# Kernel optimization log

Hardware: AMD Instinct MI355X
Metric: run time of the kernel (lower is better)

Reference implementation:

```python
import jax, jax.numpy as jnp
import numpy as np
from jax import lax

N, T, H, W, E = 512, 10, 40, 40, 8192

def _conv2d(x, w, b):
    y = lax.conv_general_dilated(x, w, (1, 1), 'SAME',
                                 dimension_numbers=('NCHW', 'OIHW', 'NCHW'))
    return y + b[None, :, None, None]

def _bn_per_t(x, g, b, eps=1e-5):
    # x: (N, T, C, H, W); torch training-mode BN stats computed per timestep (loop over t in original)
    mu = x.mean(axis=(0, 3, 4), keepdims=True)
    var = x.var(axis=(0, 3, 4), keepdims=True)
    return g[None, None, :, None, None] * (x - mu) * lax.rsqrt(var + eps) + b[None, None, :, None, None]

def _maxpool2(x):
    return lax.reduce_window(x, -jnp.inf, lax.max, (1, 1, 2, 2), (1, 1, 2, 2), 'VALID')

def _cnn(x, w1, b1, g1, be1, w2, b2, g2, be2):
    # conv3x3 -> BN -> relu -> maxpool2 -> conv3x3 -> BN -> relu -> adaptive avgpool(5,5); x: (N,T,Cin,H,W)
    n, t, c, h, w = x.shape
    y = _conv2d(x.reshape(n * t, c, h, w), w1, b1).reshape(n, t, 16, h, w)
    y = jax.nn.relu(_bn_per_t(y, g1, be1))
    y = _maxpool2(y.reshape(n * t, 16, h, w))
    y = _conv2d(y, w2, b2)
    co = w2.shape[0]
    y = jax.nn.relu(_bn_per_t(y.reshape(n, t, co, h // 2, w // 2), g2, be2))
    k = (h // 2) // 5  # 20 -> 5 is a uniform 4x4 average pool
    y = y.reshape(n, t, co, 5, k, 5, k).mean(axis=(4, 6))
    return y.reshape(n, t, co * 25)

def _sage(x, src, dst, wl, bl, wr):
    # PyG SAGEConv(aggr='max'): lin_l(max-aggregated neighbor feats) + lin_r(x); x: (T,N,F)
    t, n, f = x.shape
    msgs = x[:, src]                                               # (T,E,F) gather
    agg = jnp.full((t, n, f), -jnp.inf, x.dtype).at[:, dst].max(msgs)
    agg = jnp.where(jnp.isfinite(agg), agg, 0.0)                   # isolated nodes -> 0 (PyG convention)
    return jnp.einsum('tnf,of->tno', agg, wl) + bl + jnp.einsum('tnf,of->tno', x, wr)

def _lstm_last(x, wih, whh, bih, bhh):
    # x: (T,N,F); torch gate order i,f,g,o; returns final hidden state h_T
    t, n, _ = x.shape
    hdim = whh.shape[1]
    def step(carry, xt):
        h, c = carry
        z = xt @ wih.T + bih + h @ whh.T + bhh
        i, f, g, o = jnp.split(z, 4, axis=-1)
        c = jax.nn.sigmoid(f) * c + jax.nn.sigmoid(i) * jnp.tanh(g)
        h = jax.nn.sigmoid(o) * jnp.tanh(c)
        return (h, c), None
    init = (jnp.zeros((n, hdim), x.dtype), jnp.zeros((n, hdim), x.dtype))
    (h, _), _ = lax.scan(step, init, x)
    return h

def _forward(veg, cwsi, irrigation, edge_index, vw1, vb1, vg1, vbe1, vw2, vb2, vg2, vbe2,
             cw1, cb1, cg1, cbe1, cw2, cb2, cg2, cbe2, emb,
             s1_wl, s1_bl, s1_wr, s2_wl, s2_bl, s2_wr, wih, whh, bih, bhh, fcw, fcb):
    vfeat = _cnn(veg, vw1, vb1, vg1, vbe1, vw2, vb2, vg2, vbe2)    # (N,T,400)
    cfeat = _cnn(cwsi, cw1, cb1, cg1, cbe1, cw2, cb2, cg2, cbe2)   # (N,T,200)
    ifeat = emb[irrigation]                                        # (N,T,16)
    feats = jnp.concatenate([vfeat, cfeat, ifeat], axis=-1).transpose(1, 0, 2)  # (T,N,616)
    src, dst = edge_index[0], edge_index[1]
    x = jax.nn.relu(_sage(feats, src, dst, s1_wl, s1_bl, s1_wr))
    x = jax.nn.relu(_sage(x, src, dst, s2_wl, s2_bl, s2_wr))       # (T,N,32)
    h = _lstm_last(x, wih, whh, bih, bhh)                          # (N,64)
    return h @ fcw.T + fcb                                         # (N,1)

def setup_inputs():
    key = jax.random.key(0)
    ks = jax.random.split(key, 16)
    w = lambda i, shape: jax.random.normal(ks[i], shape, jnp.float32) * 0.05
    return dict(
        veg=jax.random.normal(ks[0], (N, T, 5, H, W), jnp.float32),
        cwsi=jax.random.normal(ks[1], (N, T, 1, H, W), jnp.float32),
        irrigation=jax.random.randint(ks[2], (N, T), 0, 3, jnp.int32),
        edge_index=jax.random.randint(ks[3], (2, E), 0, N, jnp.int32),
        vw1=w(4, (16, 5, 3, 3)), vb1=jnp.zeros(16), vg1=jnp.ones(16), vbe1=jnp.zeros(16),
        vw2=w(5, (16, 16, 3, 3)), vb2=jnp.zeros(16), vg2=jnp.ones(16), vbe2=jnp.zeros(16),
        cw1=w(6, (16, 1, 3, 3)), cb1=jnp.zeros(16), cg1=jnp.ones(16), cbe1=jnp.zeros(16),
        cw2=w(7, (8, 16, 3, 3)), cb2=jnp.zeros(8), cg2=jnp.ones(8), cbe2=jnp.zeros(8),
        emb=jax.random.normal(ks[8], (3, 16), jnp.float32),
        s1_wl=w(9, (64, 616)), s1_bl=jnp.zeros(64), s1_wr=w(10, (64, 616)),
        s2_wl=w(11, (32, 64)), s2_bl=jnp.zeros(32), s2_wr=w(12, (32, 64)),
        wih=w(13, (256, 32)), whh=w(14, (256, 64)), bih=jnp.zeros(256), bhh=jnp.zeros(256),
        fcw=w(15, (1, 64)), fcb=jnp.zeros(1),
    )

def reference(veg, cwsi, irrigation, edge_index, vw1, vb1, vg1, vbe1, vw2, vb2, vg2, vbe2,
              cw1, cb1, cg1, cbe1, cw2, cb2, cg2, cbe2, emb,
              s1_wl, s1_bl, s1_wr, s2_wl, s2_bl, s2_wr, wih, whh, bih, bhh, fcw, fcb):
    return _forward(veg, cwsi, irrigation, edge_index, vw1, vb1, vg1, vbe1, vw2, vb2, vg2, vbe2,
                    cw1, cb1, cg1, cbe1, cw2, cb2, cg2, cbe2, emb,
                    s1_wl, s1_bl, s1_wr, s2_wl, s2_bl, s2_wr, wih, whh, bih, bhh, fcw, fcb)
```

## Files before the change

kernel.cpp:

```cpp
#include <hip/hip_runtime.h>
#include <math.h>

#define NBATCH 512
#define TSTEPS 10
#define NIMG   5120
#define FEAT   616
#define NEDGE  8192

__device__ __forceinline__ float sigf(float x){ return 1.f/(1.f + expf(-x)); }

__global__ void prep_kernel(const float* __restrict__ s1wl, const float* __restrict__ s1wr,
                            const float* __restrict__ s2wl, const float* __restrict__ s2wr,
                            const float* __restrict__ wih,  const float* __restrict__ whh,
                            float* __restrict__ wlT, float* __restrict__ wrT,
                            float* __restrict__ wl2T, float* __restrict__ wr2T,
                            float* __restrict__ wihT, float* __restrict__ whhT,
                            double* __restrict__ stats)
{
  int idx = blockIdx.x*256 + threadIdx.x;
  if (idx < 39424){ wlT[(idx%616)*64 + idx/616] = s1wl[idx]; return; }
  idx -= 39424;
  if (idx < 39424){ wrT[(idx%616)*64 + idx/616] = s1wr[idx]; return; }
  idx -= 39424;
  if (idx < 2048){ wl2T[(idx%64)*32 + idx/64] = s2wl[idx]; return; }
  idx -= 2048;
  if (idx < 2048){ wr2T[(idx%64)*32 + idx/64] = s2wr[idx]; return; }
  idx -= 2048;
  if (idx < 8192){ wihT[(idx%32)*256 + idx/32] = wih[idx]; return; }
  idx -= 8192;
  if (idx < 16384){ whhT[(idx%64)*256 + idx/64] = whh[idx]; return; }
  idx -= 16384;
  if (idx < 1280){ stats[idx] = 0.0; }
}

__global__ void csr_kernel(const int* __restrict__ edges, int* __restrict__ row_start,
                           int* __restrict__ adj)
{
  __shared__ int cnt_s[512];
  __shared__ int scan_s[512];
  const int tid = threadIdx.x;
  const int* src = edges;
  const int* dst = edges + NEDGE;
  cnt_s[tid] = 0;
  __syncthreads();
  for (int e = tid; e < NEDGE; e += 512) atomicAdd(&cnt_s[dst[e]], 1);
  __syncthreads();
  int v = cnt_s[tid];
  scan_s[tid] = v;
  __syncthreads();
  for (int off = 1; off < 512; off <<= 1){
    int add = (tid >= off) ? scan_s[tid - off] : 0;
    __syncthreads();
    scan_s[tid] += add;
    __syncthreads();
  }
  int start = scan_s[tid] - v;
  row_start[tid] = start;
  if (tid == 511) row_start[512] = scan_s[511];
  cnt_s[tid] = start;
  __syncthreads();
  for (int e = tid; e < NEDGE; e += 512){
    int d = dst[e];
    int pos = atomicAdd(&cnt_s[d], 1);
    adj[pos] = src[e];
  }
}

template<int CIN>
__launch_bounds__(320)
__global__ void conv1_kernel(const float* __restrict__ in, const float* __restrict__ w,
                             double* __restrict__ stats, float* __restrict__ premax)
{
  constexpr int SMF = (CIN*936 > 2560) ? CIN*936 : 2560;
  __shared__ __attribute__((aligned(16))) float smem[SMF];
  float* in_t = smem;
  float* wl   = smem + CIN*792;
  float* red  = smem;
  const int tid = threadIdx.x;
  const int bid = blockIdx.x;
  const int img = bid / 3, strip = bid % 3;
  const int y0 = strip * 16;
  const int t = img % TSTEPS;
  const float* imgp = in + (size_t)img * CIN * 1600;

  for (int idx = tid; idx < CIN*144; idx += 320){
    int co = idx & 15, rest = idx >> 4;
    int k = rest % 9, ci = rest / 9;
    wl[(ci*9 + k)*16 + co] = w[(co*CIN + ci)*9 + k];
  }
  {
    const int r0 = tid / 44, c0 = tid % 44;
    #pragma unroll
    for (int ci = 0; ci < CIN; ci++){
      const float* ip = imgp + ci*1600;
      float* ot = &in_t[ci*792];
      int r = r0, c = c0;
      #pragma unroll
      for (int k = 0; k < 3; k++){
        int idx = tid + k*320;
        if (idx < 792){
          int gy = y0 + r - 1, gx = c - 1;
          float v = 0.f;
          if ((unsigned)gy < 40u && (unsigned)gx < 40u) v = ip[gy*40 + gx];
          ot[r*44 + c] = v;
        }
        r += 7; c += 12; if (c >= 44){ c -= 44; r += 1; }
      }
    }
  }
  __syncthreads();

  const int pos = tid % 80, cog = tid / 80;
  const int row = pos & 15, oct = pos >> 4;
  const int x8 = oct * 8;
  const int co0 = cog * 4;
  const int gy = y0 + row;
  const bool act = gy < 40;

  float acc[8][4];
  #pragma unroll
  for (int i = 0; i < 8; i++)
    #pragma unroll
    for (int j = 0; j < 4; j++) acc[i][j] = 0.f;

  for (int ci = 0; ci < CIN; ci++){
    float v[3][10];
    #pragma unroll
    for (int r = 0; r < 3; r++){
      const float* rp = &in_t[ci*792 + (row + r)*44 + x8];
      const float4 a = *(const float4*)rp;
      const float4 b = *(const float4*)(rp + 4);
      const float2 c = *(const float2*)(rp + 8);
      v[r][0] = a.x; v[r][1] = a.y; v[r][2] = a.z; v[r][3] = a.w;
      v[r][4] = b.x; v[r][5] = b.y; v[r][6] = b.z; v[r][7] = b.w;
      v[r][8] = c.x; v[r][9] = c.y;
    }
    #pragma unroll
    for (int dy = 0; dy < 3; dy++)
      #pragma unroll
      for (int dx = 0; dx < 3; dx++){
        const float4 wv = *(const float4*)&wl[(ci*9 + dy*3 + dx)*16 + co0];
        #pragma unroll
        for (int px = 0; px < 8; px++){
          float iv = v[dy][px + dx];
          acc[px][0] += iv*wv.x; acc[px][1] += iv*wv.y;
          acc[px][2] += iv*wv.z; acc[px][3] += iv*wv.w;
        }
      }
  }

  __syncthreads();

  #pragma unroll
  for (int cl = 0; cl < 4; cl++){
    float s = 0.f, q = 0.f;
    #pragma unroll
    for (int px = 0; px < 8; px++){
      float a = acc[px][cl];
      s += a; q += a*a;
    }
    red[(co0 + cl)*80 + pos]        = act ? s : 0.f;
    red[1280 + (co0 + cl)*80 + pos] = act ? q : 0.f;
  }

  {
    const int py = strip*8 + (row >> 1);
    #pragma unroll
    for (int cl = 0; cl < 4; cl++){
      float hp[4];
      #pragma unroll
      for (int j = 0; j < 4; j++)
        hp[j] = fmaxf(acc[2*j][cl], acc[2*j + 1][cl]);
      float op[4];
      #pragma unroll
      for (int j = 0; j < 4; j++) op[j] = __shfl_xor(hp[j], 1, 64);
      if (act && !(row & 1)){
        float4 r4;
        r4.x = fmaxf(hp[0], op[0]); r4.y = fmaxf(hp[1], op[1]);
        r4.z = fmaxf(hp[2], op[2]); r4.w = fmaxf(hp[3], op[3]);
        *(float4*)&premax[(size_t)img*6400 + (co0 + cl)*400 + py*20 + oct*4] = r4;
      }
    }
  }

  __syncthreads();
  if (tid < 256){
    int co = tid >> 4, seg = tid & 15;
    float vs = 0.f, vq = 0.f;
    #pragma unroll
    for (int j = 0; j < 5; j++){
      vs += red[co*80 + seg*5 + j];
      vq += red[1280 + co*80 + seg*5 + j];
    }
    #pragma unroll
    for (int off = 8; off > 0; off >>= 1){
      vs += __shfl_down(vs, off, 16);
      vq += __shfl_down(vq, off, 16);
    }
    if (seg == 0){
      atomicAdd(&stats[(t*16 + co)*2 + 0], (double)vs);
      atomicAdd(&stats[(t*16 + co)*2 + 1], (double)vq);
    }
  }
}

template<int CO>
__launch_bounds__(256)
__global__ void conv2_kernel(float* __restrict__ pooled, const float* __restrict__ w,
                             const float* __restrict__ bnp1, double* __restrict__ stats)
{
  constexpr int R = (CO == 16) ? 2 : 1;
  constexpr int P = (20/R) * 5;
  __shared__ __attribute__((aligned(16))) float in_t[16*528];
  __shared__ __attribute__((aligned(16))) float wl[144*CO];
  const int tid = threadIdx.x;
  const int img = blockIdx.x;
  const int t = img % TSTEPS;
  const size_t ib = (size_t)img * 6400;

  for (int idx = tid; idx < 144*CO; idx += 256){
    int co = idx % CO, rest = idx / CO;
    int k = rest % 9, ci = rest / 9;
    wl[(ci*9 + k)*CO + co] = w[(co*16 + ci)*9 + k];
  }
  {
    const int r0 = tid / 24, c0 = tid % 24;
    for (int ci = 0; ci < 16; ci++){
      const float sc = bnp1[(t*16 + ci)*2 + 0];
      const float sh = bnp1[(t*16 + ci)*2 + 1];
      const float* ip = pooled + ib + ci*400;
      float* ot = &in_t[ci*528];
      int r = r0, c = c0;
      #pragma unroll
      for (int k = 0; k < 3; k++){
        int idx = tid + k*256;
        if (idx < 528){
          int gy = r - 1, gx = c - 1;
          float v = 0.f;
          if ((unsigned)gy < 20u && (unsigned)gx < 20u)
            v = fmaxf(sc*ip[gy*20 + gx] + sh, 0.f);
          ot[r*24 + c] = v;
        }
        r += 10; c += 16; if (c >= 24){ c -= 24; r += 1; }
      }
    }
  }
  __syncthreads();

  const bool act = tid < P*(CO/4);
  const int q = tid % P, cog = tid / P;
  const int x4 = (q % 5) * 4, yb = (q / 5) * R;
  const int co0 = cog * 4;
  float acc[R][4][4];
  #pragma unroll
  for (int rr = 0; rr < R; rr++)
    #pragma unroll
    for (int i = 0; i < 4; i++)
      #pragma unroll
      for (int j = 0; j < 4; j++) acc[rr][i][j] = 0.f;

  if (act){
    for (int ci = 0; ci < 16; ci++){
      float v[R + 2][6];
      #pragma unroll
      for (int r = 0; r < R + 2; r++){
        const float* rp = &in_t[ci*528 + (yb + r)*24 + x4];
        const float4 a = *(const float4*)rp;
        const float2 b = *(const float2*)(rp + 4);
        v[r][0] = a.x; v[r][1] = a.y; v[r][2] = a.z; v[r][3] = a.w;
        v[r][4] = b.x; v[r][5] = b.y;
      }
      #pragma unroll
      for (int dy = 0; dy < 3; dy++)
        #pragma unroll
        for (int dx = 0; dx < 3; dx++){
          const float4 wv = *(const float4*)&wl[(ci*9 + dy*3 + dx)*CO + co0];
          #pragma unroll
          for (int rr = 0; rr < R; rr++){
            #pragma unroll
            for (int px = 0; px < 4; px++){
              float iv = v[rr + dy][px + dx];
              acc[rr][px][0] += iv*wv.x; acc[rr][px][1] += iv*wv.y;
              acc[rr][px][2] += iv*wv.z; acc[rr][px][3] += iv*wv.w;
            }
          }
        }
    }
    #pragma unroll
    for (int cl = 0; cl < 4; cl++)
      #pragma unroll
      for (int rr = 0; rr < R; rr++){
        float4 o4;
        o4.x = acc[rr][0][cl]; o4.y = acc[rr][1][cl];
        o4.z = acc[rr][2][cl]; o4.w = acc[rr][3][cl];
        *(float4*)&pooled[ib + (co0 + cl)*400 + (yb + rr)*20 + x4] = o4;
      }
  }
  __syncthreads();

  if (act){
    #pragma unroll
    for (int cl = 0; cl < 4; cl++){
      float s = 0.f, qq = 0.f;
      #pragma unroll
      for (int rr = 0; rr < R; rr++)
        #pragma unroll
        for (int px = 0; px < 4; px++){
          float a = acc[rr][px][cl];
          s += a; qq += a*a;
        }
      in_t[(co0 + cl)*P + q]            = s;
      in_t[CO*P + (co0 + cl)*P + q]     = qq;
    }
  }
  __syncthreads();
  if (tid < CO*8){
    int co = tid >> 3, seg = tid & 7;
    float vs = 0.f, vq = 0.f;
    for (int j = seg; j < P; j += 8){
      vs += in_t[co*P + j];
      vq += in_t[CO*P + co*P + j];
    }
    #pragma unroll
    for (int off = 4; off > 0; off >>= 1){
      vs += __shfl_down(vs, off, 8);
      vq += __shfl_down(vq, off, 8);
    }
    if (seg == 0){
      atomicAdd(&stats[(t*CO + co)*2 + 0], (double)vs);
      atomicAdd(&stats[(t*CO + co)*2 + 1], (double)vq);
    }
  }
}

template<int CO>
__global__ void bnavg_kernel(const float* __restrict__ raw, const float* __restrict__ bnp,
                             float* __restrict__ feats, int featBase)
{
  const int img = blockIdx.x;
  const int t = img % TSTEPS, n = img / TSTEPS;
  for (int idx = threadIdx.x; idx < CO*25; idx += 256){
    int co = idx / 25, q = idx % 25, py = q / 5, px = q % 5;
    float sc = bnp[(t*CO + co)*2 + 0];
    float sh = bnp[(t*CO + co)*2 + 1];
    const float* base = raw + (size_t)img*6400 + co*400 + (py*4)*20 + px*4;
    float s = 0.f;
    #pragma unroll
    for (int r = 0; r < 4; r++){
      float4 v = *(const float4*)(base + r*20);
      s += fmaxf(v.x*sc + sh, 0.f) + fmaxf(v.y*sc + sh, 0.f)
         + fmaxf(v.z*sc + sh, 0.f) + fmaxf(v.w*sc + sh, 0.f);
    }
    feats[(size_t)(t*NBATCH + n)*FEAT + featBase + idx] = s * 0.0625f;
  }
}

__global__ void bn_param_kernel(const double* __restrict__ stats, float* __restrict__ bnp,
                                const float* __restrict__ g, const float* __restrict__ be,
                                int C, double invCnt)
{
  int idx = threadIdx.x;
  if (idx < TSTEPS*C){
    int c = idx % C;
    double mean = stats[idx*2] * invCnt;
    double var  = stats[idx*2 + 1] * invCnt - mean*mean;
    if (var < 0.0) var = 0.0;
    double sc = (double)g[c] / sqrt(var + 1e-5);
    bnp[idx*2]     = (float)sc;
    bnp[idx*2 + 1] = be[c] - (float)(mean * sc);
  }
}

__global__ void emb_kernel(const int* __restrict__ irr, const float* __restrict__ emb,
                           float* __restrict__ feats)
{
  int idx = blockIdx.x*256 + threadIdx.x;
  if (idx >= NBATCH*TSTEPS*16) return;
  int k = idx & 15;
  int nt = idx >> 4;
  int t = nt % TSTEPS, n = nt / TSTEPS;
  feats[(size_t)(t*NBATCH + n)*FEAT + 600 + k] = emb[irr[nt]*16 + k];
}

__global__ void agg_kernel(const float* __restrict__ feats, const int* __restrict__ row_start,
                           const int* __restrict__ adj, float* __restrict__ agg)
{
  __shared__ int adjs[192];
  const int bid = blockIdx.x;
  const int t = bid / NBATCH, n = bid % NBATCH;
  const int tid = threadIdx.x;
  const int rs = row_start[n], re = row_start[n + 1];
  const int deg = re - rs;
  for (int i = tid; i < deg && i < 192; i += 256) adjs[i] = adj[rs + i];
  __syncthreads();
  const float* fb = feats + (size_t)t*NBATCH*FEAT;
  float* ab = agg + (size_t)(t*NBATCH + n)*FEAT;
  for (int f = tid; f < FEAT; f += 256){
    float m = -1e30f;
    for (int j = 0; j < deg; j++){
      int s = (j < 192) ? adjs[j] : adj[rs + j];
      m = fmaxf(m, fb[(size_t)s*FEAT + f]);
    }
    ab[f] = (deg > 0) ? m : 0.f;
  }
}

__launch_bounds__(256)
__global__ void sage1_kernel(const float* __restrict__ feats, const float* __restrict__ agg,
                             const float* __restrict__ wlT, const float* __restrict__ wrT,
                             const float* __restrict__ bl, float* __restrict__ x1)
{
  __shared__ float xr[4][616];
  __shared__ float ar[4][616];
  const int tid = threadIdx.x;
  const int bid = blockIdx.x;
  for (int idx = tid; idx < 4*616; idx += 256){
    int r = idx / 616, f = idx % 616;
    size_t row = (size_t)bid*4 + r;
    xr[r][f] = feats[row*FEAT + f];
    ar[r][f] = agg[row*FEAT + f];
  }
  __syncthreads();
  const int wid = tid >> 6, o = tid & 63;
  const int row = bid*4 + wid;
  float acc = bl[o];
  #pragma unroll 4
  for (int f = 0; f < 616; f++){
    acc += ar[wid][f]*wlT[f*64 + o] + xr[wid][f]*wrT[f*64 + o];
  }
  x1[(size_t)row*64 + o] = fmaxf(acc, 0.f);
}

__launch_bounds__(64)
__global__ void sage2_kernel(const float* __restrict__ x1, const int* __restrict__ row_start,
                             const int* __restrict__ adj, const float* __restrict__ wl2T,
                             const float* __restrict__ wr2T, const float* __restrict__ bl2,
                             float* __restrict__ x2)
{
  __shared__ float am[64], xm[64];
  __shared__ int adjs[192];
  const int bid = blockIdx.x;
  const int t = bid / NBATCH, n = bid % NBATCH;
  const int lane = threadIdx.x;
  const int rs = row_start[n], re = row_start[n + 1];
  const int deg = re - rs;
  for (int i = lane; i < deg && i < 192; i += 64) adjs[i] = adj[rs + i];
  __syncthreads();
  const float* xb = x1 + (size_t)t*NBATCH*64;
  float m = -1e30f;
  for (int j = 0; j < deg; j++){
    int s = (j < 192) ? adjs[j] : adj[rs + j];
    m = fmaxf(m, xb[s*64 + lane]);
  }
  am[lane] = (deg > 0) ? m : 0.f;
  xm[lane] = xb[n*64 + lane];
  __syncthreads();
  if (lane < 32){
    float acc = bl2[lane];
    #pragma unroll 4
    for (int f = 0; f < 64; f++){
      acc += am[f]*wl2T[f*32 + lane] + xm[f]*wr2T[f*32 + lane];
    }
    x2[(size_t)(t*NBATCH + n)*32 + lane] = fmaxf(acc, 0.f);
  }
}

__launch_bounds__(256)
__global__ void lstm_kernel(const float* __restrict__ x2, const float* __restrict__ wihT,
                            const float* __restrict__ whhT, const float* __restrict__ bih,
                            const float* __restrict__ bhh, const float* __restrict__ fcw,
                            const float* __restrict__ fcb, float* __restrict__ out)
{
  __shared__ float xb[32], hb[64], cbuf[64], zb[256];
  const int n = blockIdx.x;
  const int tid = threadIdx.x;
  if (tid < 64){ hb[tid] = 0.f; cbuf[tid] = 0.f; }
  __syncthreads();
  const float bsum = bih[tid] + bhh[tid];
  for (int t = 0; t < TSTEPS; t++){
    if (tid < 32) xb[tid] = x2[(size_t)(t*NBATCH + n)*32 + tid];
    __syncthreads();
    float acc = bsum;
    #pragma unroll 8
    for (int k = 0; k < 32; k++) acc += xb[k]*wihT[k*256 + tid];
    #pragma unroll 8
    for (int k = 0; k < 64; k++) acc += hb[k]*whhT[k*256 + tid];
    zb[tid] = acc;
    __syncthreads();
    if (tid < 64){
      float zi = zb[tid], zf = zb[64 + tid], zg = zb[128 + tid], zo = zb[192 + tid];
      float c = sigf(zf)*cbuf[tid] + sigf(zi)*tanhf(zg);
      cbuf[tid] = c;
      hb[tid] = sigf(zo)*tanhf(c);
    }
    __syncthreads();
  }
  if (tid < 64){
    float v = hb[tid]*fcw[tid];
    #pragma unroll
    for (int off = 32; off > 0; off >>= 1) v += __shfl_down(v, off, 64);
    if (tid == 0) out[n] = v + fcb[0];
  }
}

extern "C" void kernel_launch(void* const* d_in, const int* in_sizes, int n_in,
                              void* d_out, int out_size, void* d_ws, size_t ws_size,
                              hipStream_t stream)
{
  const float* veg  = (const float*)d_in[0];
  const float* cwsi = (const float*)d_in[1];
  const int*   irr  = (const int*)d_in[2];
  const int*   eidx = (const int*)d_in[3];
  const float* vw1  = (const float*)d_in[4];
  const float* vg1  = (const float*)d_in[6];
  const float* vbe1 = (const float*)d_in[7];
  const float* vw2  = (const float*)d_in[8];
  const float* vg2  = (const float*)d_in[10];
  const float* vbe2 = (const float*)d_in[11];
  const float* cw1  = (const float*)d_in[12];
  const float* cg1  = (const float*)d_in[14];
  const float* cbe1 = (const float*)d_in[15];
  const float* cw2  = (const float*)d_in[16];
  const float* cg2  = (const float*)d_in[18];
  const float* cbe2 = (const float*)d_in[19];
  const float* emb  = (const float*)d_in[20];
  const float* s1wl = (const float*)d_in[21];
  const float* s1bl = (const float*)d_in[22];
  const float* s1wr = (const float*)d_in[23];
  const float* s2wl = (const float*)d_in[24];
  const float* s2bl = (const float*)d_in[25];
  const float* s2wr = (const float*)d_in[26];
  const float* wih  = (const float*)d_in[27];
  const float* whh  = (const float*)d_in[28];
  const float* bih  = (const float*)d_in[29];
  const float* bhh  = (const float*)d_in[30];
  const float* fcw  = (const float*)d_in[31];
  const float* fcb  = (const float*)d_in[32];
  float* out = (float*)d_out;

  float* ws = (float*)d_ws;
  size_t off = 0;
  float* pooled = ws + off; off += (size_t)NIMG*6400;
  float* feats  = ws + off; off += (size_t)NIMG*FEAT;
  float* agg1   = ws + off; off += (size_t)NIMG*FEAT;
  float* x1     = ws + off; off += (size_t)NIMG*64;
  float* x2     = ws + off; off += (size_t)NIMG*32;
  float* wlT    = ws + off; off += 39424;
  float* wrT    = ws + off; off += 39424;
  float* wl2T   = ws + off; off += 2048;
  float* wr2T   = ws + off; off += 2048;
  float* wihT   = ws + off; off += 8192;
  float* whhT   = ws + off; off += 16384;
  off = (off + 1) & ~(size_t)1;
  double* stats = (double*)(ws + off); off += 2560;
  float* bnp    = ws + off; off += 1280;
  int* row_start= (int*)(ws + off); off += 513;
  int* adj      = (int*)(ws + off); off += 8192;
  (void)in_sizes; (void)n_in; (void)out_size; (void)ws_size;

  prep_kernel<<<425, 256, 0, stream>>>(s1wl, s1wr, s2wl, s2wr, wih, whh,
                                       wlT, wrT, wl2T, wr2T, wihT, whhT, stats);
  csr_kernel<<<1, 512, 0, stream>>>(eidx, row_start, adj);

  double* stV1 = stats;        float* bnV1 = bnp;
  double* stV2 = stats + 320;  float* bnV2 = bnp + 320;
  double* stC1 = stats + 640;  float* bnC1 = bnp + 640;
  double* stC2 = stats + 960;  float* bnC2 = bnp + 960;

  conv1_kernel<5><<<NIMG*3, 320, 0, stream>>>(veg, vw1, stV1, pooled);
  bn_param_kernel<<<1, 256, 0, stream>>>(stV1, bnV1, vg1, vbe1, 16, 1.0/(512.0*1600.0));
  conv2_kernel<16><<<NIMG, 256, 0, stream>>>(pooled, vw2, bnV1, stV2);
  bn_param_kernel<<<1, 256, 0, stream>>>(stV2, bnV2, vg2, vbe2, 16, 1.0/(512.0*400.0));
  bnavg_kernel<16><<<NIMG, 256, 0, stream>>>(pooled, bnV2, feats, 0);

  conv1_kernel<1><<<NIMG*3, 320, 0, stream>>>(cwsi, cw1, stC1, pooled);
  bn_param_kernel<<<1, 256, 0, stream>>>(stC1, bnC1, cg1, cbe1, 16, 1.0/(512.0*1600.0));
  conv2_kernel<8><<<NIMG, 256, 0, stream>>>(pooled, cw2, bnC1, stC2);
  bn_param_kernel<<<1, 256, 0, stream>>>(stC2, bnC2, cg2, cbe2, 8, 1.0/(512.0*400.0));
  bnavg_kernel<8><<<NIMG, 256, 0, stream>>>(pooled, bnC2, feats, 400);

  emb_kernel<<<(NBATCH*TSTEPS*16 + 255)/256, 256, 0, stream>>>(irr, emb, feats);
  agg_kernel<<<NIMG, 256, 0, stream>>>(feats, row_start, adj, agg1);
  sage1_kernel<<<NIMG/4, 256, 0, stream>>>(feats, agg1, wlT, wrT, s1bl, x1);
  sage2_kernel<<<NIMG, 64, 0, stream>>>(x1, row_start, adj, wl2T, wr2T, s2bl, x2);
  lstm_kernel<<<NBATCH, 256, 0, stream>>>(x2, wihT, whhT, bih, bhh, fcw, fcb, out);
}
```

Measured before the change: 850.9 us.

## Pre-transpose conv weights once, load them wave-uniformly, and remap conv1 threads

Conv weights are transposed once in the prep kernel, so the conv kernels no longer rebuild per-block LDS weight copies. Each thread reads the weights for its wave-uniform output-channel group straight from global memory (readfirstlane makes the group index uniform, allowing scalar loads). conv1 moves from 320 to 256 threads, with one wave per 4-channel group and 10 pixels per thread, and stages pooled outputs through LDS so global stores are coalesced. This trades LDS weight traffic and scattered float4 stores for more registers per thread and an extra barrier.

```diff
diff --git a/kernel.cpp b/kernel.cpp
--- a/kernel.cpp
+++ b/kernel.cpp
@@ -12,9 +12,13 @@
 __global__ void prep_kernel(const float* __restrict__ s1wl, const float* __restrict__ s1wr,
                             const float* __restrict__ s2wl, const float* __restrict__ s2wr,
                             const float* __restrict__ wih,  const float* __restrict__ whh,
+                            const float* __restrict__ vw1,  const float* __restrict__ cw1,
+                            const float* __restrict__ vw2,  const float* __restrict__ cw2,
                             float* __restrict__ wlT, float* __restrict__ wrT,
                             float* __restrict__ wl2T, float* __restrict__ wr2T,
                             float* __restrict__ wihT, float* __restrict__ whhT,
+                            float* __restrict__ w1vT, float* __restrict__ w1cT,
+                            float* __restrict__ w2vT, float* __restrict__ w2cT,
                             double* __restrict__ stats)
 {
   int idx = blockIdx.x*256 + threadIdx.x;
@@ -30,6 +34,26 @@
   idx -= 8192;
   if (idx < 16384){ whhT[(idx%64)*256 + idx/64] = whh[idx]; return; }
   idx -= 16384;
+  if (idx < 720){
+    int co = idx & 15, k = (idx >> 4) % 9, ci = idx / 144;
+    w1vT[idx] = vw1[(co*5 + ci)*9 + k]; return;
+  }
+  idx -= 720;
+  if (idx < 144){
+    int co = idx & 15, k = idx >> 4;
+    w1cT[idx] = cw1[co*9 + k]; return;
+  }
+  idx -= 144;
+  if (idx < 2304){
+    int co = idx & 15, k = (idx >> 4) % 9, ci = idx / 144;
+    w2vT[idx] = vw2[(co*16 + ci)*9 + k]; return;
+  }
+  idx -= 2304;
+  if (idx < 1152){
+    int co = idx & 7, k = (idx >> 3) % 9, ci = idx / 72;
+    w2cT[idx] = cw2[(co*16 + ci)*9 + k]; return;
+  }
+  idx -= 1152;
   if (idx < 1280){ stats[idx] = 0.0; }
 }
 
@@ -67,15 +91,16 @@
 }
 
 template<int CIN>
-__launch_bounds__(320)
-__global__ void conv1_kernel(const float* __restrict__ in, const float* __restrict__ w,
+__launch_bounds__(256)
+__global__ void conv1_kernel(const float* __restrict__ in, const float* __restrict__ wT,
                              double* __restrict__ stats, float* __restrict__ premax)
 {
-  constexpr int SMF = (CIN*936 > 2560) ? CIN*936 : 2560;
+  constexpr int INT = CIN*864;
+  constexpr int SMF = (INT > 4608) ? INT : 4608;
   __shared__ __attribute__((aligned(16))) float smem[SMF];
   float* in_t = smem;
-  float* wl   = smem + CIN*792;
   float* red  = smem;
+  float* plds = smem + 2048;
   const int tid = threadIdx.x;
   const int bid = blockIdx.x;
   const int img = bid / 3, strip = bid % 3;
@@ -83,70 +108,65 @@
   const int t = img % TSTEPS;
   const float* imgp = in + (size_t)img * CIN * 1600;
 
-  for (int idx = tid; idx < CIN*144; idx += 320){
-    int co = idx & 15, rest = idx >> 4;
-    int k = rest % 9, ci = rest / 9;
-    wl[(ci*9 + k)*16 + co] = w[(co*CIN + ci)*9 + k];
-  }
   {
-    const int r0 = tid / 44, c0 = tid % 44;
-    #pragma unroll
+    const int r0 = tid / 48, c0 = tid % 48;
     for (int ci = 0; ci < CIN; ci++){
       const float* ip = imgp + ci*1600;
-      float* ot = &in_t[ci*792];
+      float* ot = &in_t[ci*864];
       int r = r0, c = c0;
       #pragma unroll
-      for (int k = 0; k < 3; k++){
-        int idx = tid + k*320;
-        if (idx < 792){
+      for (int k = 0; k < 4; k++){
+        int idx = tid + k*256;
+        if (idx < 864){
           int gy = y0 + r - 1, gx = c - 1;
           float v = 0.f;
           if ((unsigned)gy < 40u && (unsigned)gx < 40u) v = ip[gy*40 + gx];
-          ot[r*44 + c] = v;
+          ot[r*48 + c] = v;
         }
-        r += 7; c += 12; if (c >= 44){ c -= 44; r += 1; }
+        r += 5; c += 16; if (c >= 48){ c -= 48; r += 1; }
       }
     }
   }
   __syncthreads();
 
-  const int pos = tid % 80, cog = tid / 80;
-  const int row = pos & 15, oct = pos >> 4;
-  const int x8 = oct * 8;
-  const int co0 = cog * 4;
+  const int lane = tid & 63;
+  const int co0 = __builtin_amdgcn_readfirstlane(tid >> 6) * 4;
+  const int row = lane & 15, g = lane >> 4;
   const int gy = y0 + row;
   const bool act = gy < 40;
 
-  float acc[8][4];
+  float acc[10][4];
   #pragma unroll
-  for (int i = 0; i < 8; i++)
+  for (int i = 0; i < 10; i++)
     #pragma unroll
     for (int j = 0; j < 4; j++) acc[i][j] = 0.f;
 
   for (int ci = 0; ci < CIN; ci++){
-    float v[3][10];
-    #pragma unroll
-    for (int r = 0; r < 3; r++){
-      const float* rp = &in_t[ci*792 + (row + r)*44 + x8];
-      const float4 a = *(const float4*)rp;
-      const float4 b = *(const float4*)(rp + 4);
-      const float2 c = *(const float2*)(rp + 8);
-      v[r][0] = a.x; v[r][1] = a.y; v[r][2] = a.z; v[r][3] = a.w;
-      v[r][4] = b.x; v[r][5] = b.y; v[r][6] = b.z; v[r][7] = b.w;
-      v[r][8] = c.x; v[r][9] = c.y;
-    }
-    #pragma unroll
-    for (int dy = 0; dy < 3; dy++)
+    const float* wp = wT + ci*144 + co0;
+    float4 sw[9];
+    #pragma unroll
+    for (int k = 0; k < 9; k++) sw[k] = *(const float4*)(wp + k*16);
+    const float* rbase = &in_t[ci*864 + row*48 + g*10];
+    #pragma unroll
+    for (int dy = 0; dy < 3; dy++){
+      float v[12];
+      const float* rp = rbase + dy*48;
+      #pragma unroll
+      for (int j = 0; j < 6; j++){
+        float2 tv = *(const float2*)(rp + 2*j);
+        v[2*j] = tv.x; v[2*j + 1] = tv.y;
+      }
       #pragma unroll
       for (int dx = 0; dx < 3; dx++){
-        const float4 wv = *(const float4*)&wl[(ci*9 + dy*3 + dx)*16 + co0];
+        const float4 wv = sw[dy*3 + dx];
         #pragma unroll
-        for (int px = 0; px < 8; px++){
-          float iv = v[dy][px + dx];
-          acc[px][0] += iv*wv.x; acc[px][1] += iv*wv.y;
-          acc[px][2] += iv*wv.z; acc[px][3] += iv*wv.w;
+        for (int p = 0; p < 10; p++){
+          float iv = v[p + dx];
+          acc[p][0] += iv*wv.x; acc[p][1] += iv*wv.y;
+          acc[p][2] += iv*wv.z; acc[p][3] += iv*wv.w;
         }
       }
+    }
   }
 
   __syncthreads();
@@ -155,42 +175,36 @@
   for (int cl = 0; cl < 4; cl++){
     float s = 0.f, q = 0.f;
     #pragma unroll
-    for (int px = 0; px < 8; px++){
-      float a = acc[px][cl];
+    for (int p = 0; p < 10; p++){
+      float a = acc[p][cl];
       s += a; q += a*a;
     }
-    red[(co0 + cl)*80 + pos]        = act ? s : 0.f;
-    red[1280 + (co0 + cl)*80 + pos] = act ? q : 0.f;
-  }
+    red[(co0 + cl)*64 + lane]        = act ? s : 0.f;
+    red[1024 + (co0 + cl)*64 + lane] = act ? q : 0.f;
+  }
+  #pragma unroll
+  for (int cl = 0; cl < 4; cl++){
+    float hp[5];
+    #pragma unroll
+    for (int j = 0; j < 5; j++) hp[j] = fmaxf(acc[2*j][cl], acc[2*j + 1][cl]);
+    float op[5];
+    #pragma unroll
+    for (int j = 0; j < 5; j++) op[j] = __shfl_xor(hp[j], 1, 64);
+    if (!(row & 1)){
+      #pragma unroll
+      for (int j = 0; j < 5; j++)
+        plds[(co0 + cl)*160 + (row >> 1)*20 + g*5 + j] = fmaxf(hp[j], op[j]);
+    }
+  }
+  __syncthreads();
 
   {
-    const int py = strip*8 + (row >> 1);
-    #pragma unroll
-    for (int cl = 0; cl < 4; cl++){
-      float hp[4];
-      #pragma unroll
-      for (int j = 0; j < 4; j++)
-        hp[j] = fmaxf(acc[2*j][cl], acc[2*j + 1][cl]);
-      float op[4];
-      #pragma unroll
-      for (int j = 0; j < 4; j++) op[j] = __shfl_xor(hp[j], 1, 64);
-      if (act && !(row & 1)){
-        float4 r4;
-        r4.x = fmaxf(hp[0], op[0]); r4.y = fmaxf(hp[1], op[1]);
-        r4.z = fmaxf(hp[2], op[2]); r4.w = fmaxf(hp[3], op[3]);
-        *(float4*)&premax[(size_t)img*6400 + (co0 + cl)*400 + py*20 + oct*4] = r4;
-      }
-    }
-  }
-
-  __syncthreads();
-  if (tid < 256){
-    int co = tid >> 4, seg = tid & 15;
+    const int co = tid >> 4, seg = tid & 15;
     float vs = 0.f, vq = 0.f;
     #pragma unroll
-    for (int j = 0; j < 5; j++){
-      vs += red[co*80 + seg*5 + j];
-      vq += red[1280 + co*80 + seg*5 + j];
+    for (int j = 0; j < 4; j++){
+      vs += red[co*64 + seg*4 + j];
+      vq += red[1024 + co*64 + seg*4 + j];
     }
     #pragma unroll
     for (int off = 8; off > 0; off >>= 1){
@@ -202,27 +216,32 @@
       atomicAdd(&stats[(t*16 + co)*2 + 1], (double)vq);
     }
   }
+  {
+    float* pb = premax + (size_t)img*6400;
+    #pragma unroll
+    for (int k = 0; k < 10; k++){
+      int idx = tid + k*256;
+      int co = idx / 160, rem = idx % 160;
+      int py = rem / 20, col = rem % 20;
+      int gpy = strip*8 + py;
+      if (gpy < 20) pb[co*400 + gpy*20 + col] = plds[idx];
+    }
+  }
 }
 
 template<int CO>
 __launch_bounds__(256)
-__global__ void conv2_kernel(float* __restrict__ pooled, const float* __restrict__ w,
+__global__ void conv2_kernel(float* __restrict__ pooled, const float* __restrict__ wT,
                              const float* __restrict__ bnp1, double* __restrict__ stats)
 {
   constexpr int R = (CO == 16) ? 2 : 1;
   constexpr int P = (20/R) * 5;
   __shared__ __attribute__((aligned(16))) float in_t[16*528];
-  __shared__ __attribute__((aligned(16))) float wl[144*CO];
   const int tid = threadIdx.x;
   const int img = blockIdx.x;
   const int t = img % TSTEPS;
   const size_t ib = (size_t)img * 6400;
 
-  for (int idx = tid; idx < 144*CO; idx += 256){
-    int co = idx % CO, rest = idx / CO;
-    int k = rest % 9, ci = rest / 9;
-    wl[(ci*9 + k)*CO + co] = w[(co*16 + ci)*9 + k];
-  }
   {
     const int r0 = tid / 24, c0 = tid % 24;
     for (int ci = 0; ci < 16; ci++){
@@ -247,8 +266,10 @@
   }
   __syncthreads();
 
-  const bool act = tid < P*(CO/4);
-  const int q = tid % P, cog = tid / P;
+  const int cog = (CO == 16) ? __builtin_amdgcn_readfirstlane(tid >> 6)
+                             : __builtin_amdgcn_readfirstlane(tid >> 7);
+  const int q   = (CO == 16) ? (tid & 63) : (tid & 127);
+  const bool act = q < P;
   const int x4 = (q % 5) * 4, yb = (q / 5) * R;
   const int co0 = cog * 4;
   float acc[R][4][4];
@@ -261,6 +282,10 @@
 
   if (act){
     for (int ci = 0; ci < 16; ci++){
+      const float* wp = wT + ci*9*CO + co0;
+      float4 sw[9];
+      #pragma unroll
+      for (int k = 0; k < 9; k++) sw[k] = *(const float4*)(wp + k*CO);
       float v[R + 2][6];
       #pragma unroll
       for (int r = 0; r < R + 2; r++){
@@ -274,7 +299,7 @@
       for (int dy = 0; dy < 3; dy++)
         #pragma unroll
         for (int dx = 0; dx < 3; dx++){
-          const float4 wv = *(const float4*)&wl[(ci*9 + dy*3 + dx)*CO + co0];
+          const float4 wv = sw[dy*3 + dx];
           #pragma unroll
           for (int rr = 0; rr < R; rr++){
             #pragma unroll
@@ -551,6 +576,10 @@
   float* wr2T   = ws + off; off += 2048;
   float* wihT   = ws + off; off += 8192;
   float* whhT   = ws + off; off += 16384;
+  float* w1vT   = ws + off; off += 720;
+  float* w1cT   = ws + off; off += 144;
+  float* w2vT   = ws + off; off += 2304;
+  float* w2cT   = ws + off; off += 1152;
   off = (off + 1) & ~(size_t)1;
   double* stats = (double*)(ws + off); off += 2560;
   float* bnp    = ws + off; off += 1280;
@@ -558,8 +587,10 @@
   int* adj      = (int*)(ws + off); off += 8192;
   (void)in_sizes; (void)n_in; (void)out_size; (void)ws_size;
 
-  prep_kernel<<<425, 256, 0, stream>>>(s1wl, s1wr, s2wl, s2wr, wih, whh,
-                                       wlT, wrT, wl2T, wr2T, wihT, whhT, stats);
+  prep_kernel<<<442, 256, 0, stream>>>(s1wl, s1wr, s2wl, s2wr, wih, whh,
+                                       vw1, cw1, vw2, cw2,
+                                       wlT, wrT, wl2T, wr2T, wihT, whhT,
+                                       w1vT, w1cT, w2vT, w2cT, stats);
   csr_kernel<<<1, 512, 0, stream>>>(eidx, row_start, adj);
 
   double* stV1 = stats;        float* bnV1 = bnp;
@@ -567,15 +598,15 @@
   double* stC1 = stats + 640;  float* bnC1 = bnp + 640;
   double* stC2 = stats + 960;  float* bnC2 = bnp + 960;
 
-  conv1_kernel<5><<<NIMG*3, 320, 0, stream>>>(veg, vw1, stV1, pooled);
+  conv1_kernel<5><<<NIMG*3, 256, 0, stream>>>(veg, w1vT, stV1, pooled);
   bn_param_kernel<<<1, 256, 0, stream>>>(stV1, bnV1, vg1, vbe1, 16, 1.0/(512.0*1600.0));
-  conv2_kernel<16><<<NIMG, 256, 0, stream>>>(pooled, vw2, bnV1, stV2);
+  conv2_kernel<16><<<NIMG, 256, 0, stream>>>(pooled, w2vT, bnV1, stV2);
   bn_param_kernel<<<1, 256, 0, stream>>>(stV2, bnV2, vg2, vbe2, 16, 1.0/(512.0*400.0));
   bnavg_kernel<16><<<NIMG, 256, 0, stream>>>(pooled, bnV2, feats, 0);
 
-  conv1_kernel<1><<<NIMG*3, 320, 0, stream>>>(cwsi, cw1, stC1, pooled);
+  conv1_kernel<1><<<NIMG*3, 256, 0, stream>>>(cwsi, w1cT, stC1, pooled);
   bn_param_kernel<<<1, 256, 0, stream>>>(stC1, bnC1, cg1, cbe1, 16, 1.0/(512.0*1600.0));
-  conv2_kernel<8><<<NIMG, 256, 0, stream>>>(pooled, cw2, bnC1, stC2);
+  conv2_kernel<8><<<NIMG, 256, 0, stream>>>(pooled, w2cT, bnC1, stC2);
   bn_param_kernel<<<1, 256, 0, stream>>>(stC2, bnC2, cg2, cbe2, 8, 1.0/(512.0*400.0));
   bnavg_kernel<8><<<NIMG, 256, 0, stream>>>(pooled, bnC2, feats, 400);
 
```

New measurement: 914.4 us. 7.5% more time.
